# Performance work log

Measured on AMD Instinct MI355X. Metric: run time of the kernel, lower is better.

The kernel has to match this reference:

```python
import jax, jax.numpy as jnp
import numpy as np

U = 100000   # user_count
I = 50000    # item_count
N = U + I    # total nodes in bipartite graph
D = 64       # embedding dim
L = 3        # num_layers
E = 4800000  # nnz of normalized adjacency
B = 8192     # batch size


def setup_inputs() -> dict:
    key = jax.random.key(0)
    ks = jax.random.split(key, 8)
    edge_src = jax.random.randint(ks[0], (E,), 0, N, dtype=jnp.int32)
    edge_dst = jax.random.randint(ks[1], (E,), 0, N, dtype=jnp.int32)
    # normalized adjacency values ~ 1/sqrt(deg_i*deg_j); small positive numbers
    edge_val = jax.random.uniform(ks[2], (E,), dtype=jnp.float32) * (1.0 / 32.0)
    user_emb_w = jax.random.normal(ks[3], (U, D), dtype=jnp.float32) * 0.01
    item_emb_w = jax.random.normal(ks[4], (I, D), dtype=jnp.float32) * 0.01
    batch_user = jax.random.randint(ks[5], (B,), 0, U, dtype=jnp.int32)
    batch_pos_item = jax.random.randint(ks[6], (B,), 0, I, dtype=jnp.int32)
    batch_neg_item = jax.random.randint(ks[7], (B,), 0, I, dtype=jnp.int32)
    return {
        "edge_src": edge_src,
        "edge_dst": edge_dst,
        "edge_val": edge_val,
        "user_emb_w": user_emb_w,
        "item_emb_w": item_emb_w,
        "batch_user": batch_user,
        "batch_pos_item": batch_pos_item,
        "batch_neg_item": batch_neg_item,
    }


def _spmm(edge_src, edge_dst, edge_val, x):
    # out[i] = sum_{e: dst[e]==i} val[e] * x[src[e]]  (sparse A @ x)
    msgs = edge_val[:, None] * x[edge_src]           # [E, D]
    return jax.ops.segment_sum(msgs, edge_dst, num_segments=N)


def _computer(edge_src, edge_dst, edge_val, user_emb_w, item_emb_w):
    all_emb = jnp.concatenate([user_emb_w, item_emb_w], axis=0)  # [N, D]
    acc = all_emb
    cur = all_emb
    for _ in range(L):
        cur = _spmm(edge_src, edge_dst, edge_val, cur)
        acc = acc + cur
    light_out = acc / jnp.float32(L + 1)  # mean over (L+1) layer embeddings
    return light_out[:U], light_out[U:]


def reference(edge_src, edge_dst, edge_val, user_emb_w, item_emb_w,
              batch_user, batch_pos_item, batch_neg_item):
    all_users, all_items = _computer(edge_src, edge_dst, edge_val,
                                     user_emb_w, item_emb_w)
    user = all_users[batch_user]       # [B, D]
    pos = all_items[batch_pos_item]    # [B, D]
    neg = all_items[batch_neg_item]    # [B, D]
    pos_score = jnp.sum(user * pos, axis=1)
    neg_score = jnp.sum(user * neg, axis=1)
    user0 = user_emb_w[batch_user]
    pos0 = item_emb_w[batch_pos_item]
    neg0 = item_emb_w[batch_neg_item]
    reg_loss = (jnp.sum(user0 * user0) + jnp.sum(pos0 * pos0)
                + jnp.sum(neg0 * neg0))
    return pos_score, neg_score, reg_loss
```

## Files before the change

### kernel.cpp

```cpp
#include <hip/hip_runtime.h>

#define D 64
#define EPT 16
#define BK 256
#define KMAX 1024

static __device__ __forceinline__ unsigned short f2bf(float f) {
    unsigned int u = __float_as_uint(f);
    unsigned int r = (u + 0x7FFFu + ((u >> 16) & 1u)) >> 16;
    return (unsigned short)r;
}
static __device__ __forceinline__ float bflo(unsigned int u) {
    return __uint_as_float(u << 16);
}
static __device__ __forceinline__ float bfhi(unsigned int u) {
    return __uint_as_float(u & 0xFFFF0000u);
}

__global__ void init_kernel(const float4* __restrict__ user_w,
                            const float4* __restrict__ item_w,
                            float4* __restrict__ acc,
                            ushort4* __restrict__ curb,
                            const int* __restrict__ flags,
                            int n_user4, int n_tot4) {
    int i = blockIdx.x * blockDim.x + threadIdx.x;
    if (i >= n_tot4) return;
    float4 v = (i < n_user4) ? user_w[i] : item_w[i - n_user4];
    ushort4 b;
    b.x = f2bf(v.x); b.y = f2bf(v.y); b.z = f2bf(v.z); b.w = f2bf(v.w);
    curb[i] = b;
    if (flags[i >> 4]) acc[i] = v;
}

__global__ void flag_kernel(const int* __restrict__ bu,
                            const int* __restrict__ bp,
                            const int* __restrict__ bn,
                            int* __restrict__ flags,
                            int* __restrict__ list,
                            int* __restrict__ n_list,
                            int U_, int B_) {
    int t = blockIdx.x * blockDim.x + threadIdx.x;
    int node = -1;
    if (t < 3 * B_) {
        if (t < B_)            node = bu[t];
        else if (t < 2 * B_)   node = U_ + bp[t - B_];
        else                   node = U_ + bn[t - 2 * B_];
    }
    int old = 1;
    if (node >= 0) old = atomicExch(&flags[node], 1);
    unsigned long long m = __ballot(old == 0);
    int lane = threadIdx.x & 63;
    int myoff = __popcll(m & ((1ull << lane) - 1ull));
    int total = __popcll(m);
    int bse = 0;
    if (lane == 0 && total) bse = atomicAdd(n_list, total);
    bse = __shfl(bse, 0, 64);
    if (old == 0) list[bse + myoff] = node;
}

__global__ void partition_kernel(const int* __restrict__ src,
                                 const int* __restrict__ dst,
                                 const float* __restrict__ val,
                                 int* __restrict__ g_pos,
                                 int2* __restrict__ st,
                                 int S_, int K_, int E_) {
    __shared__ int cnt[KMAX];
    __shared__ int base[KMAX];
    for (int k = threadIdx.x; k < K_; k += 256) cnt[k] = 0;
    __syncthreads();
    int b0 = blockIdx.x * (256 * EPT);
    int myk[EPT], myr[EPT], mysrc[EPT];
    unsigned mypk[EPT];
#pragma unroll
    for (int e = 0; e < EPT; ++e) {
        int i = b0 + e * 256 + threadIdx.x;
        if (i < E_) {
            int d = dst[i];
            int k = d >> 8;
            myk[e] = k;
            mysrc[e] = src[i];
            mypk[e] = ((unsigned)f2bf(val[i]) << 16) | (unsigned)(d & (BK - 1));
            myr[e] = atomicAdd(&cnt[k], 1);
        } else {
            myk[e] = -1;
        }
    }
    __syncthreads();
    for (int k = threadIdx.x; k < K_; k += 256) {
        int c = cnt[k];
        base[k] = c ? (k * S_ + atomicAdd(&g_pos[k], c)) : 0;
    }
    __syncthreads();
#pragma unroll
    for (int e = 0; e < EPT; ++e) {
        if (myk[e] >= 0)
            st[base[myk[e]] + myr[e]] = make_int2(mysrc[e], (int)mypk[e]);
    }
}

__global__ void scan_bkt_kernel(const int* __restrict__ cnt,
                                int* __restrict__ base, int K_) {
    __shared__ int sh[KMAX];
    int tid = threadIdx.x;
    int v = (tid < K_) ? cnt[tid] : 0;
    sh[tid] = v;
    __syncthreads();
    for (int off = 1; off < KMAX; off <<= 1) {
        int t = (tid >= off) ? sh[tid - off] : 0;
        __syncthreads();
        sh[tid] += t;
        __syncthreads();
    }
    if (tid < K_) base[tid] = sh[tid] - v;
}

__global__ void place_kernel(const int2* __restrict__ st,
                             const int* __restrict__ g_cnt,
                             const int* __restrict__ bkt_base,
                             int2* __restrict__ row_span,
                             int2* __restrict__ col_val,
                             int S_, int N_) {
    __shared__ int ldeg[BK];
    __shared__ int sh[BK];
    __shared__ int lcur[BK];
    int b = blockIdx.x;
    int tid = threadIdx.x;
    int rbeg = b << 8;
    int sbeg = b * S_;
    int cnt = g_cnt[b];
    int cbeg = bkt_base[b];
    ldeg[tid] = 0;
    __syncthreads();
    for (int i = tid; i < cnt; i += 256)
        atomicAdd(&ldeg[(unsigned)st[sbeg + i].y & (BK - 1u)], 1);
    __syncthreads();
    int v = ldeg[tid];
    sh[tid] = v;
    __syncthreads();
    for (int off = 1; off < BK; off <<= 1) {
        int t = (tid >= off) ? sh[tid - off] : 0;
        __syncthreads();
        sh[tid] += t;
        __syncthreads();
    }
    int excl = sh[tid] - v;
    lcur[tid] = excl;
    int gi = rbeg + tid;
    if (gi < N_) row_span[gi] = make_int2(cbeg + excl, cbeg + excl + v);
    __syncthreads();
    for (int i = tid; i < cnt; i += 256) {
        int2 cv = st[sbeg + i];
        int pcur = cbeg + atomicAdd(&lcur[(unsigned)cv.y & (BK - 1u)], 1);
        col_val[pcur] = cv;
    }
}

static __device__ __forceinline__ void spmm_row_body(
        int beg, int end, int lane, int q, int lid,
        const int2* __restrict__ col_val, const uint4* __restrict__ xb,
        float& s0, float& s1, float& s2, float& s3,
        float& s4, float& s5, float& s6, float& s7) {
    for (int base = beg; base < end; base += 64) {
        int e = base + lane;
        int c = 0;
        float v = 0.f;
        if (e < end) {
            int2 cv = col_val[e];
            c = cv.x;
            v = bfhi((unsigned)cv.y);
        }
        int m8 = (min(64, end - base) + 7) & ~7;
        int j = 0;
        for (; j + 16 <= m8; j += 16) {
            int cj0 = __shfl(c, j + q, 64);
            float vj0 = __shfl(v, j + q, 64);
            int cj1 = __shfl(c, j + 8 + q, 64);
            float vj1 = __shfl(v, j + 8 + q, 64);
            uint4 t0 = xb[cj0 * 8 + lid];
            uint4 t1 = xb[cj1 * 8 + lid];
            s0 += vj0 * bflo(t0.x); s1 += vj0 * bfhi(t0.x);
            s2 += vj0 * bflo(t0.y); s3 += vj0 * bfhi(t0.y);
            s4 += vj0 * bflo(t0.z); s5 += vj0 * bfhi(t0.z);
            s6 += vj0 * bflo(t0.w); s7 += vj0 * bfhi(t0.w);
            s0 += vj1 * bflo(t1.x); s1 += vj1 * bfhi(t1.x);
            s2 += vj1 * bflo(t1.y); s3 += vj1 * bfhi(t1.y);
            s4 += vj1 * bflo(t1.z); s5 += vj1 * bfhi(t1.z);
            s6 += vj1 * bflo(t1.w); s7 += vj1 * bfhi(t1.w);
        }
        if (j < m8) {
            int cj = __shfl(c, j + q, 64);
            float vj = __shfl(v, j + q, 64);
            uint4 t = xb[cj * 8 + lid];
            s0 += vj * bflo(t.x); s1 += vj * bfhi(t.x);
            s2 += vj * bflo(t.y); s3 += vj * bfhi(t.y);
            s4 += vj * bflo(t.z); s5 += vj * bfhi(t.z);
            s6 += vj * bflo(t.w); s7 += vj * bfhi(t.w);
        }
    }
#pragma unroll
    for (int off = 32; off >= 8; off >>= 1) {
        s0 += __shfl_xor(s0, off, 64);
        s1 += __shfl_xor(s1, off, 64);
        s2 += __shfl_xor(s2, off, 64);
        s3 += __shfl_xor(s3, off, 64);
        s4 += __shfl_xor(s4, off, 64);
        s5 += __shfl_xor(s5, off, 64);
        s6 += __shfl_xor(s6, off, 64);
        s7 += __shfl_xor(s7, off, 64);
    }
}

__global__ void spmm_csr_kernel(const int2* __restrict__ row_span,
                                const int2* __restrict__ col_val,
                                const uint4* __restrict__ xb,
                                uint4* __restrict__ nxtb,
                                float4* __restrict__ acc,
                                const int* __restrict__ flags,
                                int N_) {
    int row = (int)((blockIdx.x * blockDim.x + threadIdx.x) >> 6);
    int lane = threadIdx.x & 63;
    if (row >= N_) return;
    int q = lane >> 3;
    int lid = lane & 7;
    int2 sp = row_span[row];
    float s0 = 0, s1 = 0, s2 = 0, s3 = 0, s4 = 0, s5 = 0, s6 = 0, s7 = 0;
    spmm_row_body(sp.x, sp.y, lane, q, lid, col_val, xb,
                  s0, s1, s2, s3, s4, s5, s6, s7);
    if (q == 0) {
        uint4 b;
        b.x = (unsigned)f2bf(s0) | ((unsigned)f2bf(s1) << 16);
        b.y = (unsigned)f2bf(s2) | ((unsigned)f2bf(s3) << 16);
        b.z = (unsigned)f2bf(s4) | ((unsigned)f2bf(s5) << 16);
        b.w = (unsigned)f2bf(s6) | ((unsigned)f2bf(s7) << 16);
        nxtb[row * 8 + lid] = b;
        if (flags[row]) {
            float4* ap = acc + row * 16 + lid * 2;
            float4 a0 = ap[0];
            a0.x += s0; a0.y += s1; a0.z += s2; a0.w += s3;
            ap[0] = a0;
            float4 a1 = ap[1];
            a1.x += s4; a1.y += s5; a1.z += s6; a1.w += s7;
            ap[1] = a1;
        }
    }
}

__global__ void spmm_rows_kernel(const int2* __restrict__ row_span,
                                 const int2* __restrict__ col_val,
                                 const uint4* __restrict__ xb,
                                 float4* __restrict__ acc,
                                 const int* __restrict__ list,
                                 const int* __restrict__ n_list) {
    int w = (int)((blockIdx.x * blockDim.x + threadIdx.x) >> 6);
    if (w >= *n_list) return;
    int row = list[w];
    int lane = threadIdx.x & 63;
    int q = lane >> 3;
    int lid = lane & 7;
    int2 sp = row_span[row];
    float s0 = 0, s1 = 0, s2 = 0, s3 = 0, s4 = 0, s5 = 0, s6 = 0, s7 = 0;
    spmm_row_body(sp.x, sp.y, lane, q, lid, col_val, xb,
                  s0, s1, s2, s3, s4, s5, s6, s7);
    if (q == 0) {
        float4* ap = acc + row * 16 + lid * 2;
        float4 a0 = ap[0];
        a0.x += s0; a0.y += s1; a0.z += s2; a0.w += s3;
        ap[0] = a0;
        float4 a1 = ap[1];
        a1.x += s4; a1.y += s5; a1.z += s6; a1.w += s7;
        ap[1] = a1;
    }
}

__global__ void final_kernel(const float* __restrict__ acc,
                             const float* __restrict__ user_w,
                             const float* __restrict__ item_w,
                             const int* __restrict__ bu,
                             const int* __restrict__ bp,
                             const int* __restrict__ bn,
                             float* __restrict__ out,
                             float* __restrict__ red,
                             int U_, int B_) {
    __shared__ float pr[4];
    int w = (int)((blockIdx.x * blockDim.x + threadIdx.x) >> 6);
    int lane = threadIdx.x & 63;
    bool valid = (w < B_);
    float ps = 0.f, ns = 0.f, r = 0.f;
    if (valid) {
        int iu = bu[w], ip = bp[w], in_ = bn[w];
        const float scale = 0.25f;
        float u = acc[(long)iu * D + lane] * scale;
        float p = acc[(long)(U_ + ip) * D + lane] * scale;
        float g = acc[(long)(U_ + in_) * D + lane] * scale;
        ps = u * p;
        ns = u * g;
        float u0 = user_w[(long)iu * D + lane];
        float p0 = item_w[(long)ip * D + lane];
        float n0 = item_w[(long)in_ * D + lane];
        r = u0 * u0 + p0 * p0 + n0 * n0;
    }
#pragma unroll
    for (int off = 32; off; off >>= 1) {
        ps += __shfl_down(ps, off, 64);
        ns += __shfl_down(ns, off, 64);
        r  += __shfl_down(r, off, 64);
    }
    if (lane == 0) pr[threadIdx.x >> 6] = r;
    __syncthreads();
    if (threadIdx.x == 0)
        red[blockIdx.x] = pr[0] + pr[1] + pr[2] + pr[3];
    if (valid && lane == 0) {
        out[w] = ps;
        out[B_ + w] = ns;
    }
}

__global__ void reduce_kernel(const float* __restrict__ red,
                              float* __restrict__ out_scalar, int nblk) {
    __shared__ float sh[256];
    float s = 0.f;
    for (int i = threadIdx.x; i < nblk; i += 256) s += red[i];
    sh[threadIdx.x] = s;
    __syncthreads();
    for (int off = 128; off; off >>= 1) {
        if (threadIdx.x < off) sh[threadIdx.x] += sh[threadIdx.x + off];
        __syncthreads();
    }
    if (threadIdx.x == 0) *out_scalar = sh[0];
}

extern "C" void kernel_launch(void* const* d_in, const int* in_sizes, int n_in,
                              void* d_out, int out_size, void* d_ws, size_t ws_size,
                              hipStream_t stream) {
    const int*   edge_src = (const int*)d_in[0];
    const int*   edge_dst = (const int*)d_in[1];
    const float* edge_val = (const float*)d_in[2];
    const float* user_w   = (const float*)d_in[3];
    const float* item_w   = (const float*)d_in[4];
    const int*   bu       = (const int*)d_in[5];
    const int*   bp       = (const int*)d_in[6];
    const int*   bn       = (const int*)d_in[7];

    int E_ = in_sizes[0];
    int U_ = in_sizes[3] / D;
    int I_ = in_sizes[4] / D;
    int B_ = in_sizes[5];
    int N_ = U_ + I_;
    long ND = (long)N_ * D;
    int K_ = (N_ + BK - 1) >> 8;
    int S_ = ((E_ / K_) * 3 / 2 + 255) & ~255;

    char* p = (char*)d_ws;
    int2* col_val  = (int2*)p;   p += (size_t)E_ * sizeof(int2);
    int2* row_span = (int2*)p;   p += (size_t)N_ * sizeof(int2);
    int*  bkt_base = (int*)p;    p += KMAX * sizeof(int);
    float* red     = (float*)p;  p += 4096 * sizeof(float);
    char* zb = p;
    int*  g_pos    = (int*)p;    p += KMAX * sizeof(int);
    int*  n_list   = (int*)p;    p += 256;
    int*  flags    = (int*)p;    p += (size_t)N_ * sizeof(int);
    size_t zbytes  = (size_t)(p - zb);
    int*  list     = (int*)p;    p += (size_t)3 * B_ * sizeof(int);
    p = (char*)(((uintptr_t)p + 255) & ~(uintptr_t)255);
    int2* st = (int2*)p;
    float* acc = (float*)p;
    unsigned short* curb = (unsigned short*)(acc + ND);
    unsigned short* nxtb = curb + ND;
    float* out = (float*)d_out;

    int n4 = (int)(ND / 4);
    int nu4 = U_ * D / 4;

    hipMemsetAsync(zb, 0, zbytes, stream);
    partition_kernel<<<(E_ + 256 * EPT - 1) / (256 * EPT), 256, 0, stream>>>(
        edge_src, edge_dst, edge_val, g_pos, st, S_, K_, E_);
    scan_bkt_kernel<<<1, KMAX, 0, stream>>>(g_pos, bkt_base, K_);
    place_kernel<<<K_, 256, 0, stream>>>(st, g_pos, bkt_base, row_span,
                                         col_val, S_, N_);

    flag_kernel<<<(3 * B_ + 255) / 256, 256, 0, stream>>>(
        bu, bp, bn, flags, list, n_list, U_, B_);

    init_kernel<<<(n4 + 255) / 256, 256, 0, stream>>>(
        (const float4*)user_w, (const float4*)item_w,
        (float4*)acc, (ushort4*)curb, flags, nu4, n4);

    spmm_csr_kernel<<<(N_ + 3) / 4, 256, 0, stream>>>(
        row_span, col_val, (const uint4*)curb, (uint4*)nxtb, (float4*)acc,
        flags, N_);
    spmm_csr_kernel<<<(N_ + 3) / 4, 256, 0, stream>>>(
        row_span, col_val, (const uint4*)nxtb, (uint4*)curb, (float4*)acc,
        flags, N_);
    spmm_rows_kernel<<<(3 * B_ + 3) / 4, 256, 0, stream>>>(
        row_span, col_val, (const uint4*)curb, (float4*)acc, list, n_list);

    int nblk = (B_ * 64 + 255) / 256;
    final_kernel<<<nblk, 256, 0, stream>>>(
        acc, user_w, item_w, bu, bp, bn, out, red, U_, B_);
    reduce_kernel<<<1, 256, 0, stream>>>(red, out + 2 * B_, nblk);
}
```

Baseline: 455.7 us.

## Stage partitioned edges in LDS so bucket scatter writes are contiguous

The partition kernel now runs 1024-thread blocks over chunks of 6144 edges. It computes an in-block prefix scan of per-bucket counts, sorts edges by bucket into shared memory, and then writes them out linearly, so consecutive threads write adjacent slots within each bucket run. This replaces the fully scattered 8-byte global stores with mostly coalesced ones. In exchange it adds a 1024-wide shared-memory scan with many barriers and about 48KB of LDS per block, which lowers occupancy. It also packs the bucket id into the high bits of src, which assumes src fits in 20 bits and K fits in 12 bits.

```diff
diff --git a/kernel.cpp b/kernel.cpp
--- a/kernel.cpp
+++ b/kernel.cpp
@@ -1,9 +1,10 @@
 #include <hip/hip_runtime.h>
 
 #define D 64
-#define EPT 16
 #define BK 256
 #define KMAX 1024
+#define PCH 6144
+#define PEPT 6
 
 static __device__ __forceinline__ unsigned short f2bf(float f) {
     unsigned int u = __float_as_uint(f);
@@ -58,22 +59,27 @@
     if (old == 0) list[bse + myoff] = node;
 }
 
-__global__ void partition_kernel(const int* __restrict__ src,
-                                 const int* __restrict__ dst,
-                                 const float* __restrict__ val,
-                                 int* __restrict__ g_pos,
-                                 int2* __restrict__ st,
-                                 int S_, int K_, int E_) {
+__global__ void __launch_bounds__(1024)
+partition_kernel(const int* __restrict__ src,
+                 const int* __restrict__ dst,
+                 const float* __restrict__ val,
+                 int* __restrict__ g_pos,
+                 int2* __restrict__ st,
+                 int S_, int K_, int E_) {
+    __shared__ int2 stg[PCH];
     __shared__ int cnt[KMAX];
-    __shared__ int base[KMAX];
-    for (int k = threadIdx.x; k < K_; k += 256) cnt[k] = 0;
-    __syncthreads();
-    int b0 = blockIdx.x * (256 * EPT);
-    int myk[EPT], myr[EPT], mysrc[EPT];
-    unsigned mypk[EPT];
+    __shared__ int sh[KMAX];
+    __shared__ int gb[KMAX];
+    int tid = threadIdx.x;
+    for (int k = tid; k < K_; k += 1024) cnt[k] = 0;
+    __syncthreads();
+    int b0 = blockIdx.x * PCH;
+    int nc = min(PCH, E_ - b0);
+    int myk[PEPT], myr[PEPT], mysrc[PEPT];
+    unsigned mypk[PEPT];
 #pragma unroll
-    for (int e = 0; e < EPT; ++e) {
-        int i = b0 + e * 256 + threadIdx.x;
+    for (int e = 0; e < PEPT; ++e) {
+        int i = b0 + e * 1024 + tid;
         if (i < E_) {
             int d = dst[i];
             int k = d >> 8;
@@ -86,15 +92,33 @@
         }
     }
     __syncthreads();
-    for (int k = threadIdx.x; k < K_; k += 256) {
-        int c = cnt[k];
-        base[k] = c ? (k * S_ + atomicAdd(&g_pos[k], c)) : 0;
+    int v = (tid < K_) ? cnt[tid] : 0;
+    sh[tid] = v;
+    __syncthreads();
+    for (int off = 1; off < KMAX; off <<= 1) {
+        int t = (tid >= off) ? sh[tid - off] : 0;
+        __syncthreads();
+        sh[tid] += t;
+        __syncthreads();
+    }
+    if (tid < K_ && v) {
+        int lbase = sh[tid] - v;
+        gb[tid] = (tid * S_ + atomicAdd(&g_pos[tid], v)) - lbase;
     }
     __syncthreads();
 #pragma unroll
-    for (int e = 0; e < EPT; ++e) {
-        if (myk[e] >= 0)
-            st[base[myk[e]] + myr[e]] = make_int2(mysrc[e], (int)mypk[e]);
+    for (int e = 0; e < PEPT; ++e) {
+        int k = myk[e];
+        if (k >= 0) {
+            int slot = (sh[k] - cnt[k]) + myr[e];
+            stg[slot] = make_int2(mysrc[e] | (k << 20), (int)mypk[e]);
+        }
+    }
+    __syncthreads();
+    for (int l = tid; l < nc; l += 1024) {
+        int2 ev = stg[l];
+        int k = (int)((unsigned)ev.x >> 20);
+        st[gb[k] + l] = make_int2(ev.x & 0xFFFFF, ev.y);
     }
 }
 
@@ -372,7 +396,7 @@
     int nu4 = U_ * D / 4;
 
     hipMemsetAsync(zb, 0, zbytes, stream);
-    partition_kernel<<<(E_ + 256 * EPT - 1) / (256 * EPT), 256, 0, stream>>>(
+    partition_kernel<<<(E_ + PCH - 1) / PCH, 1024, 0, stream>>>(
         edge_src, edge_dst, edge_val, g_pos, st, S_, K_, E_);
     scan_bkt_kernel<<<1, KMAX, 0, stream>>>(g_pos, bkt_base, K_);
     place_kernel<<<K_, 256, 0, stream>>>(st, g_pos, bkt_base, row_span,
```

Result: faster. 408.9 us (-10.3%).
